# Kernel tuning notes

Hardware: AMD Instinct MI355X
Metric: run time of the kernel (lower is better)

The kernel has to match this reference:

```python
import jax, jax.numpy as jnp
import numpy as np

N_NODES = 50000
N_EDGES = 640000
D = 128
L = 3


def setup_inputs() -> dict:
    key = jax.random.key(0)
    k1, k2, k3, k4 = jax.random.split(key, 4)
    x = jax.random.normal(k1, (N_NODES, D), dtype=jnp.float32)
    # Glorot-ish scale so activations stay O(1) across 3 layers
    Ws = jax.random.normal(k2, (L, D, D), dtype=jnp.float32) * (1.0 / np.sqrt(D))
    bs = jnp.zeros((L, D), dtype=jnp.float32)
    edge_src = jax.random.randint(k3, (N_EDGES,), 0, N_NODES, dtype=jnp.int32)
    edge_dst = jax.random.randint(k4, (N_EDGES,), 0, N_NODES, dtype=jnp.int32)
    return {"x": x, "Ws": Ws, "bs": bs, "edge_src": edge_src, "edge_dst": edge_dst}


def reference(x, Ws, bs, edge_src, edge_dst):
    n = x.shape[0]
    ones = jnp.ones(edge_src.shape[0], dtype=x.dtype)
    # degrees, clamped to 1 as in dgl GraphConv(norm='both')
    deg_out = jnp.maximum(jax.ops.segment_sum(ones, edge_src, num_segments=n), 1.0)
    deg_in = jnp.maximum(jax.ops.segment_sum(ones, edge_dst, num_segments=n), 1.0)
    inv_sqrt_out = jax.lax.rsqrt(deg_out)[:, None]  # [N,1]
    inv_sqrt_in = jax.lax.rsqrt(deg_in)[:, None]    # [N,1]
    for l in range(Ws.shape[0]):
        h = x * inv_sqrt_out                         # src normalization
        msg = h[edge_src]                            # [E,D] gather
        agg = jax.ops.segment_sum(msg, edge_dst, num_segments=n)  # [N,D] scatter-add
        h = agg * inv_sqrt_in                        # dst normalization
        x = jax.nn.relu(h @ Ws[l] + bs[l])           # linear + ReLU
    return x
```

## Files before the change

kernel.cpp:

```cpp
#include <hip/hip_runtime.h>
#include <hip/hip_fp16.h>

typedef __attribute__((ext_vector_type(8))) _Float16 half8;
typedef __attribute__((ext_vector_type(4))) float f32x4;
typedef unsigned int u32;
typedef unsigned short u16;
typedef unsigned long long u64;

#define ELL_PAD 64
#define BKT 128
#define BKT_SH 7
#define EPB 2048
#define NAMAX 512


__global__ __launch_bounds__(256) void initpack(int* __restrict__ deg_out,
                                                u32* __restrict__ xz0,
                                                u32* __restrict__ xz1,
                                                const float* __restrict__ Ws,
                                                _Float16* __restrict__ Whi,
                                                _Float16* __restrict__ Wlo,
                                                int N, int padU32, int zb, int packTotal) {
  int b = blockIdx.x;
  if (b < zb) {
    int i = b * 256 + threadIdx.x;
    if (i < N) deg_out[i] = 0;
    if (b == 0) {
      for (int j = threadIdx.x; j < padU32; j += 256) { xz0[j] = 0; xz1[j] = 0; }
    }
    return;
  }
  int i = (b - zb) * 256 + threadIdx.x;
  if (i < packTotal) {
    int lane  = i & 63;
    int kstep = (i >> 6) & 3;
    int ntile = (i >> 8) & 7;
    int layer = i >> 11;
    int nn = ntile * 16 + (lane & 15);
    int k0 = kstep * 32 + (lane >> 4) * 8;
    const float* W = Ws + (size_t)layer * 128 * 128;
    size_t base = (size_t)i * 8;
    for (int j = 0; j < 8; j++) {
      float v = W[(k0 + j) * 128 + nn];
      _Float16 hi = (_Float16)v;
      Whi[base + j] = hi;
      Wlo[base + j] = (_Float16)(v - (float)hi);
    }
  }
}


__global__ __launch_bounds__(256) void parta(const int* __restrict__ esrc,
                                             const int* __restrict__ edst,
                                             int* __restrict__ deg_out,
                                             u32* __restrict__ part,
                                             u32* __restrict__ runTab,
                                             int E, int NB) {
  __shared__ u32 hist[1024];
  __shared__ u32 stage[EPB];
  int a = blockIdx.x;
  int e0 = a * EPB;
  int e1 = min(E, e0 + EPB);
  int len = e1 - e0;
  for (int j = threadIdx.x; j <= NB; j += 256) hist[j] = 0;
  __syncthreads();
  for (int i = e0 + threadIdx.x; i < e1; i += 256) {
    int s = esrc[i];
    int d = edst[i];
    atomicAdd(&deg_out[s], 1);
    atomicAdd(&hist[d >> BKT_SH], 1u);
  }
  __syncthreads();
  if (threadIdx.x == 0) {
    u32 run = 0;
    for (int b = 0; b < NB; b++) { u32 t = hist[b]; hist[b] = run; run += t; }
  }
  __syncthreads();
  u32* rt = runTab + (size_t)a * (NB + 1);
  for (int b = threadIdx.x; b < NB; b += 256) rt[b] = hist[b];
  if (threadIdx.x == 0) rt[NB] = (u32)len;
  __syncthreads();
  for (int i = e0 + threadIdx.x; i < e1; i += 256) {
    int s = esrc[i];
    int d = edst[i];
    u32 p = atomicAdd(&hist[d >> BKT_SH], 1u);
    stage[p] = (u32)s | ((u32)(d & (BKT - 1)) << 16);
  }
  __syncthreads();
  u32* op = part + (size_t)a * EPB;
  for (int j = threadIdx.x; j < len; j += 256) op[j] = stage[j];
}


__global__ __launch_bounds__(256) void partb(const u32* __restrict__ part,
                                             const u32* __restrict__ runTab,
                                             int* __restrict__ deg_in,
                                             u16* __restrict__ ell,
                                             int N, int NA, int NB) {
  __shared__ u16 slice[BKT * ELL_PAD];
  __shared__ u32 cnt[BKT];
  __shared__ u32 roff[NAMAX + 1];
  __shared__ u32 rbase[NAMAX];
  int b = blockIdx.x;
  int base = b * BKT;
  int hi = min(BKT, N - base);
  if (hi <= 0) return;

  u32 nv = ((u32)N << 16) | (u32)N;
  u32* s32 = (u32*)slice;
  for (int j = threadIdx.x; j < BKT * (ELL_PAD / 2); j += 256) s32[j] = nv;
  for (int j = threadIdx.x; j < BKT; j += 256) cnt[j] = 0;
  for (int a = threadIdx.x; a < NA; a += 256) {
    u32 s = runTab[(size_t)a * (NB + 1) + b];
    u32 e = runTab[(size_t)a * (NB + 1) + b + 1];
    roff[a]  = e - s;
    rbase[a] = (u32)a * EPB + s;
  }
  __syncthreads();
  if (threadIdx.x == 0) {
    u32 run = 0;
    for (int a = 0; a < NA; a++) { u32 t = roff[a]; roff[a] = run; run += t; }
    roff[NA] = run;
  }
  __syncthreads();
  int T = (int)roff[NA];
  for (int i = threadIdx.x; i < T; i += 256) {
    int lo = 0, hh = NA;
    while (hh - lo > 1) {
      int mid = (lo + hh) >> 1;
      if (roff[mid] <= (u32)i) lo = mid; else hh = mid;
    }
    u32 pair = part[(size_t)rbase[lo] + ((u32)i - roff[lo])];
    u32 dl  = pair >> 16;
    u32 src = pair & 0xFFFFu;
    u32 c = atomicAdd(&cnt[dl], 1u);
    if (c < ELL_PAD) slice[dl * ELL_PAD + c] = (u16)src;
  }
  __syncthreads();
  for (int t = threadIdx.x; t < hi; t += 256) deg_in[base + t] = (int)cnt[t];
  u32* eg = (u32*)(ell + (size_t)base * ELL_PAD);
  for (int j = threadIdx.x; j < hi * (ELL_PAD / 2); j += 256) eg[j] = s32[j];
}


__global__ __launch_bounds__(256) void xscale(const float* __restrict__ x,
                                              const int* __restrict__ deg_out,
                                              __half2* __restrict__ xh, int n64) {
  int gid = blockIdx.x * 256 + threadIdx.x;
  if (gid >= n64) return;
  int row = gid >> 6;
  int d = deg_out[row]; if (d < 1) d = 1;
  float s = rsqrtf((float)d);
  float2 v = ((const float2*)x)[gid];
  xh[gid] = __floats2half2_rn(v.x * s, v.y * s);
}


__global__ __launch_bounds__(512) void layer16(const _Float16* __restrict__ xh,
                                               const int* __restrict__ deg_in,
                                               const u16* __restrict__ ell,
                                               const _Float16* __restrict__ Whi,
                                               const _Float16* __restrict__ Wlo,
                                               const float* __restrict__ bias,
                                               const int* __restrict__ deg_out,
                                               __half* __restrict__ out16,
                                               float* __restrict__ out32, int n) {
  __shared__ _Float16 As[16 * 136];
  const int wave = threadIdx.x >> 6;
  const int lane = threadIdx.x & 63;
  const int sub  = lane & 15;
  const int grp  = lane >> 4;
  const int sh   = grp << 4;
  const u32 sub16 = (u32)sub * 16u;
  const int rowBase = blockIdx.x * 16;
  const char* __restrict__ xb = (const char*)xh;

  {
    int r0 = rowBase + wave * 2, r1 = r0 + 1;
    int d0 = (r0 < n) ? deg_in[r0] : 0;
    int d1 = (r1 < n) ? deg_in[r1] : 0;
    int l0 = d0 > ELL_PAD ? ELL_PAD : d0;
    int l1 = d1 > ELL_PAD ? ELL_PAD : d1;
    int t0 = (l0 + 3) & ~3;
    int t1 = (l1 + 3) & ~3;
    const u16* ep0 = ell + (u32)(r0 < n ? r0 : 0) * ELL_PAD;
    const u16* ep1 = ell + (u32)(r1 < n ? r1 : 0) * ELL_PAD;

    float a0[8] = {0.f, 0.f, 0.f, 0.f, 0.f, 0.f, 0.f, 0.f};
    float a1[8] = {0.f, 0.f, 0.f, 0.f, 0.f, 0.f, 0.f, 0.f};

    int m = t0 < t1 ? t0 : t1;
    int e = 0;
    for (; e + 8 <= m; e += 8) {
      u64 wa0 = *(const u64*)&ep0[e];
      u64 wa1 = *(const u64*)&ep0[e + 4];
      u64 wb0 = *(const u64*)&ep1[e];
      u64 wb1 = *(const u64*)&ep1[e + 4];
      u32 ia0 = ((u32)(wa0 >> sh) & 0xFFFFu) * 256u + sub16;
      u32 ia1 = ((u32)(wa1 >> sh) & 0xFFFFu) * 256u + sub16;
      u32 ib0 = ((u32)(wb0 >> sh) & 0xFFFFu) * 256u + sub16;
      u32 ib1 = ((u32)(wb1 >> sh) & 0xFFFFu) * 256u + sub16;
      half8 va0 = *(const half8*)(xb + ia0);
      half8 va1 = *(const half8*)(xb + ia1);
      half8 vb0 = *(const half8*)(xb + ib0);
      half8 vb1 = *(const half8*)(xb + ib1);
#pragma unroll
      for (int j = 0; j < 8; j++) {
        a0[j] += (float)va0[j] + (float)va1[j];
        a1[j] += (float)vb0[j] + (float)vb1[j];
      }
    }
    for (; e < m; e += 4) {
      u64 wa = *(const u64*)&ep0[e];
      u64 wb = *(const u64*)&ep1[e];
      u32 ia = ((u32)(wa >> sh) & 0xFFFFu) * 256u + sub16;
      u32 ib = ((u32)(wb >> sh) & 0xFFFFu) * 256u + sub16;
      half8 va = *(const half8*)(xb + ia);
      half8 vb = *(const half8*)(xb + ib);
#pragma unroll
      for (int j = 0; j < 8; j++) { a0[j] += (float)va[j]; a1[j] += (float)vb[j]; }
    }
    for (int ea = m; ea < t0; ea += 4) {
      u64 wa = *(const u64*)&ep0[ea];
      u32 ia = ((u32)(wa >> sh) & 0xFFFFu) * 256u + sub16;
      half8 va = *(const half8*)(xb + ia);
#pragma unroll
      for (int j = 0; j < 8; j++) a0[j] += (float)va[j];
    }
    for (int eb = m; eb < t1; eb += 4) {
      u64 wb = *(const u64*)&ep1[eb];
      u32 ib = ((u32)(wb >> sh) & 0xFFFFu) * 256u + sub16;
      half8 vb = *(const half8*)(xb + ib);
#pragma unroll
      for (int j = 0; j < 8; j++) a1[j] += (float)vb[j];
    }

#pragma unroll
    for (int j = 0; j < 8; j++) {
      a0[j] += __shfl_xor(a0[j], 16, 64);
      a0[j] += __shfl_xor(a0[j], 32, 64);
      a1[j] += __shfl_xor(a1[j], 16, 64);
      a1[j] += __shfl_xor(a1[j], 32, 64);
    }

    float si0 = rsqrtf((float)(d0 < 1 ? 1 : d0));
    float si1 = rsqrtf((float)(d1 < 1 ? 1 : d1));
    if (grp == 0) {
      half8 h0, h1;
#pragma unroll
      for (int j = 0; j < 8; j++) {
        h0[j] = (_Float16)(a0[j] * si0);
        h1[j] = (_Float16)(a1[j] * si1);
      }
      *(half8*)&As[(wave * 2 + 0) * 136 + sub * 8] = h0;
      *(half8*)&As[(wave * 2 + 1) * 136 + sub * 8] = h1;
    }
  }
  __syncthreads();

  f32x4 acc = (f32x4){0.f, 0.f, 0.f, 0.f};
#pragma unroll
  for (int ks = 0; ks < 4; ks++) {
    half8 a  = *(const half8*)&As[(size_t)sub * 136 + ks * 32 + grp * 8];
    half8 bh = *(const half8*)&Whi[((wave * 4 + ks) * 64 + lane) * 8];
    half8 bl = *(const half8*)&Wlo[((wave * 4 + ks) * 64 + lane) * 8];
    acc = __builtin_amdgcn_mfma_f32_16x16x32_f16(a, bh, acc, 0, 0, 0);
    acc = __builtin_amdgcn_mfma_f32_16x16x32_f16(a, bl, acc, 0, 0, 0);
  }

  const int r0c = rowBase + grp * 4;
  const int col = wave * 16 + sub;
  const float bv = bias[col];
#pragma unroll
  for (int r = 0; r < 4; r++) {
    int row = r0c + r;
    if (row < n) {
      float v = fmaxf(acc[r] + bv, 0.f);
      if (out16) {
        int d = deg_out[row]; if (d < 1) d = 1;
        out16[(size_t)row * 128 + col] = __float2half(v * rsqrtf((float)d));
      } else {
        out32[(size_t)row * 128 + col] = v;
      }
    }
  }
}


extern "C" void kernel_launch(void* const* d_in, const int* in_sizes, int n_in,
                              void* d_out, int out_size, void* d_ws, size_t ws_size,
                              hipStream_t stream) {
  const float* x   = (const float*)d_in[0];
  const float* Ws  = (const float*)d_in[1];
  const float* bs  = (const float*)d_in[2];
  const int* esrc  = (const int*)d_in[3];
  const int* edst  = (const int*)d_in[4];

  const int D = 128;
  const int N = in_sizes[0] / D;
  const int E = in_sizes[3];
  const int L = in_sizes[1] / (D * D);
  const int Npad = ((N + 15) / 16) * 16;
  const int NA = (E + EPB - 1) / EPB;
  const int NB = (N + BKT - 1) / BKT;

  char* base = (char*)d_ws;
  size_t off = 0;
  auto alloc = [&](size_t bytes) {
    char* p = base + off;
    off = (off + bytes + 255) & ~(size_t)255;
    return p;
  };
  int*      deg_out = (int*)alloc((size_t)N * 4);
  int*      deg_in  = (int*)alloc((size_t)N * 4);
  u16*      ell     = (u16*)alloc((size_t)N * ELL_PAD * 2);
  _Float16* Whi     = (_Float16*)alloc((size_t)L * 16384 * 2);
  _Float16* Wlo     = (_Float16*)alloc((size_t)L * 16384 * 2);
  _Float16* xh0     = (_Float16*)alloc((size_t)(Npad + 16) * 128 * 2);
  _Float16* xh1     = (_Float16*)alloc((size_t)(Npad + 16) * 128 * 2);
  u32*      part    = (u32*)alloc((size_t)NA * EPB * 4);
  u32*      runTab  = (u32*)alloc((size_t)NA * (NB + 1) * 4);

  const int zb = (N + 255) / 256;
  const int packTotal = L * 2048;
  const int packB = (packTotal + 255) / 256;
  const int padU32 = 16 * 64;

  initpack<<<dim3(zb + packB), dim3(256), 0, stream>>>(
      deg_out,
      (u32*)(xh0 + (size_t)N * 128), (u32*)(xh1 + (size_t)N * 128),
      Ws, Whi, Wlo, N, padU32, zb, packTotal);
  parta<<<dim3(NA), dim3(256), 0, stream>>>(
      esrc, edst, deg_out, part, runTab, E, NB);
  partb<<<dim3(NB), dim3(256), 0, stream>>>(
      part, runTab, deg_in, ell, N, NA, NB);
  xscale<<<dim3((N * 64 + 255) / 256), dim3(256), 0, stream>>>(
      x, deg_out, (__half2*)xh0, N * 64);

  float* outf = (float*)d_out;
  _Float16* ping[2] = {xh0, xh1};
  const dim3 lgrid(Npad / 16), lblk(512);

  for (int l = 0; l < L; l++) {
    bool last = (l == L - 1);
    layer16<<<lgrid, lblk, 0, stream>>>(
        (const _Float16*)ping[l & 1], deg_in, ell,
        Whi + (size_t)l * 16384, Wlo + (size_t)l * 16384,
        bs + (size_t)l * D, deg_out,
        last ? nullptr : (__half*)ping[(l + 1) & 1],
        last ? outf : nullptr, N);
  }
}
```

Before: 250.8 us.

## Widen layer tiles to 32 rows and parallelize partition scans

The fused aggregate+GEMM kernel now handles 32 rows per block, with each wave gathering four rows and each MFMA wave running two row tiles. This reuses the W fragments across two tiles and puts more independent gather loads in flight. The partition kernels move to 512 threads and replace serial single-thread prefix scans with parallel Hillis-Steele scans. partb also adds a shared run-id table that replaces the per-edge binary search. The costs are higher register pressure from four accumulator sets and fewer blocks in the layer kernel.

```diff
diff --git a/kernel.cpp b/kernel.cpp
--- a/kernel.cpp
+++ b/kernel.cpp
@@ -12,6 +12,7 @@
 #define BKT_SH 7
 #define EPB 2048
 #define NAMAX 512
+#define RUNCAP 3072
 
 
 __global__ __launch_bounds__(256) void initpack(int* __restrict__ deg_out,
@@ -50,37 +51,44 @@
 }
 
 
-__global__ __launch_bounds__(256) void parta(const int* __restrict__ esrc,
+__global__ __launch_bounds__(512) void parta(const int* __restrict__ esrc,
                                              const int* __restrict__ edst,
                                              int* __restrict__ deg_out,
                                              u32* __restrict__ part,
                                              u32* __restrict__ runTab,
                                              int E, int NB) {
-  __shared__ u32 hist[1024];
+  __shared__ u32 hist[512];
   __shared__ u32 stage[EPB];
+  __shared__ u32 scanA[512];
   int a = blockIdx.x;
   int e0 = a * EPB;
   int e1 = min(E, e0 + EPB);
   int len = e1 - e0;
-  for (int j = threadIdx.x; j <= NB; j += 256) hist[j] = 0;
-  __syncthreads();
-  for (int i = e0 + threadIdx.x; i < e1; i += 256) {
+  int tid = threadIdx.x;
+  if (tid <= NB) hist[tid] = 0;
+  __syncthreads();
+  for (int i = e0 + tid; i < e1; i += 512) {
     int s = esrc[i];
     int d = edst[i];
     atomicAdd(&deg_out[s], 1);
     atomicAdd(&hist[d >> BKT_SH], 1u);
   }
   __syncthreads();
-  if (threadIdx.x == 0) {
-    u32 run = 0;
-    for (int b = 0; b < NB; b++) { u32 t = hist[b]; hist[b] = run; run += t; }
-  }
-  __syncthreads();
+  u32 myc = (tid < NB) ? hist[tid] : 0;
+  scanA[tid] = myc;
+  __syncthreads();
+  for (int off = 1; off < NB; off <<= 1) {
+    u32 t = scanA[tid] + ((tid >= off) ? scanA[tid - off] : 0);
+    __syncthreads();
+    scanA[tid] = t;
+    __syncthreads();
+  }
+  u32 excl = scanA[tid] - myc;
   u32* rt = runTab + (size_t)a * (NB + 1);
-  for (int b = threadIdx.x; b < NB; b += 256) rt[b] = hist[b];
-  if (threadIdx.x == 0) rt[NB] = (u32)len;
-  __syncthreads();
-  for (int i = e0 + threadIdx.x; i < e1; i += 256) {
+  if (tid < NB) { rt[tid] = excl; hist[tid] = excl; }
+  if (tid == 0) rt[NB] = (u32)len;
+  __syncthreads();
+  for (int i = e0 + tid; i < e1; i += 512) {
     int s = esrc[i];
     int d = edst[i];
     u32 p = atomicAdd(&hist[d >> BKT_SH], 1u);
@@ -88,11 +96,11 @@
   }
   __syncthreads();
   u32* op = part + (size_t)a * EPB;
-  for (int j = threadIdx.x; j < len; j += 256) op[j] = stage[j];
-}
-
-
-__global__ __launch_bounds__(256) void partb(const u32* __restrict__ part,
+  for (int j = tid; j < len; j += 512) op[j] = stage[j];
+}
+
+
+__global__ __launch_bounds__(512) void partb(const u32* __restrict__ part,
                                              const u32* __restrict__ runTab,
                                              int* __restrict__ deg_in,
                                              u16* __restrict__ ell,
@@ -101,45 +109,61 @@
   __shared__ u32 cnt[BKT];
   __shared__ u32 roff[NAMAX + 1];
   __shared__ u32 rbase[NAMAX];
+  __shared__ u16 runid[RUNCAP];
+  __shared__ u32 scanA[512];
   int b = blockIdx.x;
   int base = b * BKT;
   int hi = min(BKT, N - base);
   if (hi <= 0) return;
+  int tid = threadIdx.x;
 
   u32 nv = ((u32)N << 16) | (u32)N;
   u32* s32 = (u32*)slice;
-  for (int j = threadIdx.x; j < BKT * (ELL_PAD / 2); j += 256) s32[j] = nv;
-  for (int j = threadIdx.x; j < BKT; j += 256) cnt[j] = 0;
-  for (int a = threadIdx.x; a < NA; a += 256) {
-    u32 s = runTab[(size_t)a * (NB + 1) + b];
-    u32 e = runTab[(size_t)a * (NB + 1) + b + 1];
-    roff[a]  = e - s;
-    rbase[a] = (u32)a * EPB + s;
-  }
-  __syncthreads();
-  if (threadIdx.x == 0) {
-    u32 run = 0;
-    for (int a = 0; a < NA; a++) { u32 t = roff[a]; roff[a] = run; run += t; }
-    roff[NA] = run;
-  }
+  for (int j = tid; j < BKT * (ELL_PAD / 2); j += 512) s32[j] = nv;
+  if (tid < BKT) cnt[tid] = 0;
+  u32 mylen = 0;
+  if (tid < NA) {
+    u32 s = runTab[(size_t)tid * (NB + 1) + b];
+    u32 e = runTab[(size_t)tid * (NB + 1) + b + 1];
+    mylen = e - s;
+    rbase[tid] = (u32)tid * EPB + s;
+  }
+  scanA[tid] = mylen;
+  __syncthreads();
+  for (int off = 1; off < NA + 1; off <<= 1) {
+    u32 t = scanA[tid] + ((tid >= off) ? scanA[tid - off] : 0);
+    __syncthreads();
+    scanA[tid] = t;
+    __syncthreads();
+  }
+  if (tid <= NA) roff[tid] = scanA[tid] - mylen;
   __syncthreads();
   int T = (int)roff[NA];
-  for (int i = threadIdx.x; i < T; i += 256) {
-    int lo = 0, hh = NA;
-    while (hh - lo > 1) {
-      int mid = (lo + hh) >> 1;
-      if (roff[mid] <= (u32)i) lo = mid; else hh = mid;
-    }
-    u32 pair = part[(size_t)rbase[lo] + ((u32)i - roff[lo])];
+  for (int a = tid; a < NA; a += 512) {
+    u32 s0 = roff[a];
+    u32 l  = roff[a + 1] - s0;
+    for (u32 k = 0; k < l; k++)
+      if (s0 + k < RUNCAP) runid[s0 + k] = (u16)a;
+  }
+  __syncthreads();
+  for (int i = tid; i < T; i += 512) {
+    int a;
+    if (i < RUNCAP) a = runid[i];
+    else {
+      int lo = 0, hh = NA;
+      while (hh - lo > 1) { int mid = (lo + hh) >> 1; if (roff[mid] <= (u32)i) lo = mid; else hh = mid; }
+      a = lo;
+    }
+    u32 pair = part[(size_t)rbase[a] + ((u32)i - roff[a])];
     u32 dl  = pair >> 16;
     u32 src = pair & 0xFFFFu;
     u32 c = atomicAdd(&cnt[dl], 1u);
     if (c < ELL_PAD) slice[dl * ELL_PAD + c] = (u16)src;
   }
   __syncthreads();
-  for (int t = threadIdx.x; t < hi; t += 256) deg_in[base + t] = (int)cnt[t];
+  for (int t = tid; t < hi; t += 512) deg_in[base + t] = (int)cnt[t];
   u32* eg = (u32*)(ell + (size_t)base * ELL_PAD);
-  for (int j = threadIdx.x; j < hi * (ELL_PAD / 2); j += 256) eg[j] = s32[j];
+  for (int j = tid; j < hi * (ELL_PAD / 2); j += 512) eg[j] = s32[j];
 }
 
 
@@ -156,7 +180,7 @@
 }
 
 
-__global__ __launch_bounds__(512) void layer16(const _Float16* __restrict__ xh,
+__global__ __launch_bounds__(512) void layer32(const _Float16* __restrict__ xh,
                                                const int* __restrict__ deg_in,
                                                const u16* __restrict__ ell,
                                                const _Float16* __restrict__ Whi,
@@ -165,122 +189,116 @@
                                                const int* __restrict__ deg_out,
                                                __half* __restrict__ out16,
                                                float* __restrict__ out32, int n) {
-  __shared__ _Float16 As[16 * 136];
+  __shared__ _Float16 As[32 * 136];
   const int wave = threadIdx.x >> 6;
   const int lane = threadIdx.x & 63;
   const int sub  = lane & 15;
   const int grp  = lane >> 4;
-  const int sh   = grp << 4;
   const u32 sub16 = (u32)sub * 16u;
-  const int rowBase = blockIdx.x * 16;
+  const int rowBase = blockIdx.x * 32;
   const char* __restrict__ xb = (const char*)xh;
 
   {
-    int r0 = rowBase + wave * 2, r1 = r0 + 1;
-    int d0 = (r0 < n) ? deg_in[r0] : 0;
-    int d1 = (r1 < n) ? deg_in[r1] : 0;
-    int l0 = d0 > ELL_PAD ? ELL_PAD : d0;
-    int l1 = d1 > ELL_PAD ? ELL_PAD : d1;
-    int t0 = (l0 + 3) & ~3;
-    int t1 = (l1 + 3) & ~3;
-    const u16* ep0 = ell + (u32)(r0 < n ? r0 : 0) * ELL_PAD;
-    const u16* ep1 = ell + (u32)(r1 < n ? r1 : 0) * ELL_PAD;
-
-    float a0[8] = {0.f, 0.f, 0.f, 0.f, 0.f, 0.f, 0.f, 0.f};
-    float a1[8] = {0.f, 0.f, 0.f, 0.f, 0.f, 0.f, 0.f, 0.f};
-
-    int m = t0 < t1 ? t0 : t1;
-    int e = 0;
-    for (; e + 8 <= m; e += 8) {
-      u64 wa0 = *(const u64*)&ep0[e];
-      u64 wa1 = *(const u64*)&ep0[e + 4];
-      u64 wb0 = *(const u64*)&ep1[e];
-      u64 wb1 = *(const u64*)&ep1[e + 4];
-      u32 ia0 = ((u32)(wa0 >> sh) & 0xFFFFu) * 256u + sub16;
-      u32 ia1 = ((u32)(wa1 >> sh) & 0xFFFFu) * 256u + sub16;
-      u32 ib0 = ((u32)(wb0 >> sh) & 0xFFFFu) * 256u + sub16;
-      u32 ib1 = ((u32)(wb1 >> sh) & 0xFFFFu) * 256u + sub16;
-      half8 va0 = *(const half8*)(xb + ia0);
-      half8 va1 = *(const half8*)(xb + ia1);
-      half8 vb0 = *(const half8*)(xb + ib0);
-      half8 vb1 = *(const half8*)(xb + ib1);
+    int r[4], d[4], t[4];
+    const u16* ep[4];
+    int minT = 0x7fffffff, maxT = 0;
+#pragma unroll
+    for (int q = 0; q < 4; q++) {
+      r[q] = rowBase + wave * 4 + q;
+      d[q] = (r[q] < n) ? deg_in[r[q]] : 0;
+      int l = d[q] > ELL_PAD ? ELL_PAD : d[q];
+      t[q] = (l + 3) & ~3;
+      ep[q] = ell + (u32)(r[q] < n ? r[q] : 0) * ELL_PAD;
+      minT = t[q] < minT ? t[q] : minT;
+      maxT = t[q] > maxT ? t[q] : maxT;
+    }
+
+    float acc[4][8];
+#pragma unroll
+    for (int q = 0; q < 4; q++)
+#pragma unroll
+      for (int j = 0; j < 8; j++) acc[q][j] = 0.f;
+
+    int mAll = minT & ~7;
+    for (int e = 0; e + 8 <= mAll + 8 && e < mAll; e += 8) {
+#pragma unroll
+      for (int q = 0; q < 4; q++) {
+        uint4 iw = *(const uint4*)&ep[q][e];
+        u32 w0 = (grp & 2) ? iw.y : iw.x;
+        u32 w1 = (grp & 2) ? iw.w : iw.z;
+        u32 i0 = ((grp & 1) ? (w0 >> 16) : (w0 & 0xFFFFu)) * 256u + sub16;
+        u32 i1 = ((grp & 1) ? (w1 >> 16) : (w1 & 0xFFFFu)) * 256u + sub16;
+        half8 v0 = *(const half8*)(xb + i0);
+        half8 v1 = *(const half8*)(xb + i1);
+#pragma unroll
+        for (int j = 0; j < 8; j++) acc[q][j] += (float)v0[j] + (float)v1[j];
+      }
+    }
+    for (int e = mAll; e < maxT; e += 4) {
+#pragma unroll
+      for (int q = 0; q < 4; q++) {
+        if (e < t[q]) {
+          u64 w = *(const u64*)&ep[q][e];
+          u32 i0 = ((u32)(w >> (grp << 4)) & 0xFFFFu) * 256u + sub16;
+          half8 v = *(const half8*)(xb + i0);
+#pragma unroll
+          for (int j = 0; j < 8; j++) acc[q][j] += (float)v[j];
+        }
+      }
+    }
+
+#pragma unroll
+    for (int q = 0; q < 4; q++)
 #pragma unroll
       for (int j = 0; j < 8; j++) {
-        a0[j] += (float)va0[j] + (float)va1[j];
-        a1[j] += (float)vb0[j] + (float)vb1[j];
-      }
-    }
-    for (; e < m; e += 4) {
-      u64 wa = *(const u64*)&ep0[e];
-      u64 wb = *(const u64*)&ep1[e];
-      u32 ia = ((u32)(wa >> sh) & 0xFFFFu) * 256u + sub16;
-      u32 ib = ((u32)(wb >> sh) & 0xFFFFu) * 256u + sub16;
-      half8 va = *(const half8*)(xb + ia);
-      half8 vb = *(const half8*)(xb + ib);
-#pragma unroll
-      for (int j = 0; j < 8; j++) { a0[j] += (float)va[j]; a1[j] += (float)vb[j]; }
-    }
-    for (int ea = m; ea < t0; ea += 4) {
-      u64 wa = *(const u64*)&ep0[ea];
-      u32 ia = ((u32)(wa >> sh) & 0xFFFFu) * 256u + sub16;
-      half8 va = *(const half8*)(xb + ia);
-#pragma unroll
-      for (int j = 0; j < 8; j++) a0[j] += (float)va[j];
-    }
-    for (int eb = m; eb < t1; eb += 4) {
-      u64 wb = *(const u64*)&ep1[eb];
-      u32 ib = ((u32)(wb >> sh) & 0xFFFFu) * 256u + sub16;
-      half8 vb = *(const half8*)(xb + ib);
-#pragma unroll
-      for (int j = 0; j < 8; j++) a1[j] += (float)vb[j];
-    }
-
-#pragma unroll
-    for (int j = 0; j < 8; j++) {
-      a0[j] += __shfl_xor(a0[j], 16, 64);
-      a0[j] += __shfl_xor(a0[j], 32, 64);
-      a1[j] += __shfl_xor(a1[j], 16, 64);
-      a1[j] += __shfl_xor(a1[j], 32, 64);
-    }
-
-    float si0 = rsqrtf((float)(d0 < 1 ? 1 : d0));
-    float si1 = rsqrtf((float)(d1 < 1 ? 1 : d1));
+        acc[q][j] += __shfl_xor(acc[q][j], 16, 64);
+        acc[q][j] += __shfl_xor(acc[q][j], 32, 64);
+      }
+
     if (grp == 0) {
-      half8 h0, h1;
-#pragma unroll
-      for (int j = 0; j < 8; j++) {
-        h0[j] = (_Float16)(a0[j] * si0);
-        h1[j] = (_Float16)(a1[j] * si1);
-      }
-      *(half8*)&As[(wave * 2 + 0) * 136 + sub * 8] = h0;
-      *(half8*)&As[(wave * 2 + 1) * 136 + sub * 8] = h1;
-    }
-  }
-  __syncthreads();
-
-  f32x4 acc = (f32x4){0.f, 0.f, 0.f, 0.f};
+#pragma unroll
+      for (int q = 0; q < 4; q++) {
+        float si = rsqrtf((float)(d[q] < 1 ? 1 : d[q]));
+        half8 h;
+#pragma unroll
+        for (int j = 0; j < 8; j++) h[j] = (_Float16)(acc[q][j] * si);
+        *(half8*)&As[(wave * 4 + q) * 136 + sub * 8] = h;
+      }
+    }
+  }
+  __syncthreads();
+
+  f32x4 acc0 = (f32x4){0.f, 0.f, 0.f, 0.f};
+  f32x4 acc1 = (f32x4){0.f, 0.f, 0.f, 0.f};
 #pragma unroll
   for (int ks = 0; ks < 4; ks++) {
-    half8 a  = *(const half8*)&As[(size_t)sub * 136 + ks * 32 + grp * 8];
     half8 bh = *(const half8*)&Whi[((wave * 4 + ks) * 64 + lane) * 8];
     half8 bl = *(const half8*)&Wlo[((wave * 4 + ks) * 64 + lane) * 8];
-    acc = __builtin_amdgcn_mfma_f32_16x16x32_f16(a, bh, acc, 0, 0, 0);
-    acc = __builtin_amdgcn_mfma_f32_16x16x32_f16(a, bl, acc, 0, 0, 0);
-  }
-
-  const int r0c = rowBase + grp * 4;
+    half8 a0 = *(const half8*)&As[(size_t)sub * 136 + ks * 32 + grp * 8];
+    half8 a1 = *(const half8*)&As[(size_t)(16 + sub) * 136 + ks * 32 + grp * 8];
+    acc0 = __builtin_amdgcn_mfma_f32_16x16x32_f16(a0, bh, acc0, 0, 0, 0);
+    acc0 = __builtin_amdgcn_mfma_f32_16x16x32_f16(a0, bl, acc0, 0, 0, 0);
+    acc1 = __builtin_amdgcn_mfma_f32_16x16x32_f16(a1, bh, acc1, 0, 0, 0);
+    acc1 = __builtin_amdgcn_mfma_f32_16x16x32_f16(a1, bl, acc1, 0, 0, 0);
+  }
+
   const int col = wave * 16 + sub;
   const float bv = bias[col];
 #pragma unroll
-  for (int r = 0; r < 4; r++) {
-    int row = r0c + r;
-    if (row < n) {
-      float v = fmaxf(acc[r] + bv, 0.f);
-      if (out16) {
-        int d = deg_out[row]; if (d < 1) d = 1;
-        out16[(size_t)row * 128 + col] = __float2half(v * rsqrtf((float)d));
-      } else {
-        out32[(size_t)row * 128 + col] = v;
+  for (int rt = 0; rt < 2; rt++) {
+    f32x4 av = rt ? acc1 : acc0;
+    int r0c = rowBase + rt * 16 + grp * 4;
+#pragma unroll
+    for (int rr = 0; rr < 4; rr++) {
+      int row = r0c + rr;
+      if (row < n) {
+        float v = fmaxf(av[rr] + bv, 0.f);
+        if (out16) {
+          int dg = deg_out[row]; if (dg < 1) dg = 1;
+          out16[(size_t)row * 128 + col] = __float2half(v * rsqrtf((float)dg));
+        } else {
+          out32[(size_t)row * 128 + col] = v;
+        }
       }
     }
   }
@@ -300,7 +318,7 @@
   const int N = in_sizes[0] / D;
   const int E = in_sizes[3];
   const int L = in_sizes[1] / (D * D);
-  const int Npad = ((N + 15) / 16) * 16;
+  const int Npad = ((N + 31) / 32) * 32;
   const int NA = (E + EPB - 1) / EPB;
   const int NB = (N + BKT - 1) / BKT;
 
@@ -330,20 +348,20 @@
       deg_out,
       (u32*)(xh0 + (size_t)N * 128), (u32*)(xh1 + (size_t)N * 128),
       Ws, Whi, Wlo, N, padU32, zb, packTotal);
-  parta<<<dim3(NA), dim3(256), 0, stream>>>(
+  parta<<<dim3(NA), dim3(512), 0, stream>>>(
       esrc, edst, deg_out, part, runTab, E, NB);
-  partb<<<dim3(NB), dim3(256), 0, stream>>>(
+  partb<<<dim3(NB), dim3(512), 0, stream>>>(
       part, runTab, deg_in, ell, N, NA, NB);
   xscale<<<dim3((N * 64 + 255) / 256), dim3(256), 0, stream>>>(
       x, deg_out, (__half2*)xh0, N * 64);
 
   float* outf = (float*)d_out;
   _Float16* ping[2] = {xh0, xh1};
-  const dim3 lgrid(Npad / 16), lblk(512);
+  const dim3 lgrid(Npad / 32), lblk(512);
 
   for (int l = 0; l < L; l++) {
     bool last = (l == L - 1);
-    layer16<<<lgrid, lblk, 0, stream>>>(
+    layer32<<<lgrid, lblk, 0, stream>>>(
         (const _Float16*)ping[l & 1], deg_in, ell,
         Whi + (size_t)l * 16384, Wlo + (size_t)l * 16384,
         bs + (size_t)l * D, deg_out,
```

New measurement: 277.8 us. 10.8% more time.
